# Optimization experiments

Hardware: AMD Instinct MI355X
Metric: run time of the kernel (lower is better)

Reference implementation:

```python
import jax, jax.numpy as jnp
import numpy as np

N, E, F_IN = 50000, 800000, 128
H1, C1 = 4, 32          # layer 1: heads, channels (concat -> 128)
H2, C2 = 1, 40          # layer 2: out heads, num_class (mean over heads)
NEG_SLOPE = 0.2


def setup_inputs() -> dict:
    key = jax.random.key(0)
    ks = jax.random.split(key, 10)
    x = jax.random.normal(ks[0], (N, F_IN), dtype=jnp.float32)
    edge_index = jax.random.randint(ks[1], (2, E), 0, N, dtype=jnp.int32)
    s1 = 1.0 / np.sqrt(F_IN)
    s2 = 1.0 / np.sqrt(H1 * C1)
    W1 = jax.random.normal(ks[2], (F_IN, H1 * C1), dtype=jnp.float32) * s1
    att_src1 = jax.random.normal(ks[3], (H1, C1), dtype=jnp.float32) * s1
    att_dst1 = jax.random.normal(ks[4], (H1, C1), dtype=jnp.float32) * s1
    b1 = jnp.zeros((H1 * C1,), dtype=jnp.float32)
    W2 = jax.random.normal(ks[5], (H1 * C1, H2 * C2), dtype=jnp.float32) * s2
    att_src2 = jax.random.normal(ks[6], (H2, C2), dtype=jnp.float32) * s2
    att_dst2 = jax.random.normal(ks[7], (H2, C2), dtype=jnp.float32) * s2
    b2 = jnp.zeros((C2,), dtype=jnp.float32)
    return {"x": x, "edge_index": edge_index, "W1": W1, "att_src1": att_src1,
            "att_dst1": att_dst1, "b1": b1, "W2": W2, "att_src2": att_src2,
            "att_dst2": att_dst2, "b2": b2}


def _gat_layer(x, src, dst, W, a_src, a_dst, b, concat):
    # PyG GATConv (eval): linear -> per-head attention logits on edges ->
    # segment-softmax over each destination's in-edges -> scatter-aggregate.
    n = x.shape[0]
    Hh, C = a_src.shape
    h = (x @ W).reshape(n, Hh, C)                       # [N,H,C]
    al_s = jnp.sum(h * a_src, axis=-1)                  # [N,H]
    al_d = jnp.sum(h * a_dst, axis=-1)                  # [N,H]
    alpha = jax.nn.leaky_relu(al_s[src] + al_d[dst], NEG_SLOPE)  # [E,H]
    m = jax.lax.stop_gradient(jax.ops.segment_max(alpha, dst, num_segments=n))
    e = jnp.exp(alpha - m[dst])
    denom = jax.ops.segment_sum(e, dst, num_segments=n)
    a = e / (denom[dst] + 1e-16)                        # [E,H]
    out = jax.ops.segment_sum(h[src] * a[..., None], dst, num_segments=n)
    out = out.reshape(n, Hh * C) if concat else out.mean(axis=1)
    return out + b


def reference(x, edge_index, W1, att_src1, att_dst1, b1, W2, att_src2, att_dst2, b2):
    n = x.shape[0]
    loop = jnp.arange(n, dtype=edge_index.dtype)        # GATConv add_self_loops=True
    src = jnp.concatenate([edge_index[0], loop])
    dst = jnp.concatenate([edge_index[1], loop])
    h = _gat_layer(x, src, dst, W1, att_src1, att_dst1, b1, concat=True)
    h = jax.nn.elu(h)
    out = _gat_layer(h, src, dst, W2, att_src2, att_dst2, b2, concat=False)
    return out
```

## Files before the change

kernel.cpp:

```cpp
#include <hip/hip_runtime.h>
#include <hip/hip_bf16.h>
#include <hip/hip_fp16.h>
#include <math.h>

constexpr int N_NODES = 50000;
constexpr int E_EDGES = 800000;
constexpr float NEG_SLOPE = 0.2f;
constexpr int CAP = 64;
constexpr int G1_BLOCKS   = (N_NODES + 63) / 64;
constexpr int LINK_CHUNKS = (E_EDGES + 2047) / 2048;
constexpr int LINK_BLOCKS = LINK_CHUNKS * 8;
constexpr int RANGE_SZ    = N_NODES / 8;

typedef _Float16 half8 __attribute__((ext_vector_type(8)));
typedef _Float16 half2v __attribute__((ext_vector_type(2)));
typedef float    floatx4 __attribute__((ext_vector_type(4)));

static inline int cdiv(long long a, int b) { return (int)((a + b - 1) / b); }

__device__ inline float leaky(float a) { return a > 0.f ? a : NEG_SLOPE * a; }
__device__ inline unsigned pack2h(float a, float b) {
    union { _Float16 h[2]; unsigned u; } p;
    p.h[0] = (_Float16)a; p.h[1] = (_Float16)b; return p.u;
}
__device__ inline float2 unp2h(unsigned u) {
    __half2 hh = *reinterpret_cast<__half2*>(&u);
    return __half22float2(hh);
}
__device__ inline float sel4(const float4& v, int h) {
    float a = (h & 2) ? v.z : v.x;
    float b = (h & 2) ? v.w : v.y;
    return (h & 1) ? b : a;
}

__global__ __launch_bounds__(256) void prep_kernel(const float* __restrict__ W1,
                                                   const float* __restrict__ W2,
                                                   int* __restrict__ deg,
                                                   _Float16* __restrict__ w1t,
                                                   _Float16* __restrict__ w2t) {
    int b = blockIdx.x, t = threadIdx.x;
    if (b < 196) {
        int i = b * 256 + t;
        if (i < N_NODES) deg[i] = 0;
        return;
    }
    if (b < 196 + 64) {
        int idx = (b - 196) * 256 + t;
        int k = idx >> 7, c = idx & 127;
        w1t[c * 128 + k] = (_Float16)W1[k * 128 + c];
        return;
    }
    {
        int idx = (b - 260) * 256 + t;
        int k = idx / 40, c = idx - k * 40;
        w2t[c * 128 + k] = (_Float16)W2[k * 40 + c];
    }
}

__global__ __launch_bounds__(256, 8) void gemm1_link_kernel(const float* __restrict__ x,
                                                            const _Float16* __restrict__ w1t,
                                                            const float* __restrict__ as1,
                                                            const float* __restrict__ ad1,
                                                            unsigned short* __restrict__ h1h,
                                                            float* __restrict__ als,
                                                            float* __restrict__ ald,
                                                            const int* __restrict__ ei,
                                                            int* __restrict__ deg,
                                                            unsigned short* __restrict__ csr16) {
    __shared__ _Float16 xS[64 * 136];
    __shared__ float asld[128], adld[128];
    int t = threadIdx.x;

    if (blockIdx.x >= G1_BLOCKS) {
        int lb    = blockIdx.x - G1_BLOCKS;
        int range = lb & 7;
        int chunk = lb >> 3;
        int e0    = chunk * 2048 + t * 8;
        if (e0 < E_EDGES) {
            int4 sa = *(const int4*)&ei[e0];
            int4 sb = *(const int4*)&ei[e0 + 4];
            int4 da = *(const int4*)&ei[E_EDGES + e0];
            int4 db = *(const int4*)&ei[E_EDGES + e0 + 4];
            int ss[8] = { sa.x, sa.y, sa.z, sa.w, sb.x, sb.y, sb.z, sb.w };
            int dd[8] = { da.x, da.y, da.z, da.w, db.x, db.y, db.z, db.w };
            int dlo = range * RANGE_SZ, dhi = dlo + RANGE_SZ;
            #pragma unroll
            for (int j = 0; j < 8; ++j) {
                if (dd[j] >= dlo && dd[j] < dhi) {
                    int slot = atomicAdd(&deg[dd[j]], 1) + 1;
                    if (slot < CAP) csr16[dd[j] * CAP + slot] = (unsigned short)ss[j];
                }
            }
        }
        return;
    }

    int row0 = blockIdx.x * 64;
    if (t < 128) { asld[t] = as1[t]; adld[t] = ad1[t]; }
    #pragma unroll
    for (int i = 0; i < 8; ++i) {
        int fi = i * 256 + t;
        int r = fi >> 5, c4 = (fi & 31) * 4;
        int gr = row0 + r;
        float4 v = make_float4(0.f, 0.f, 0.f, 0.f);
        if (gr < N_NODES) v = *(const float4*)&x[(size_t)gr * 128 + c4];
        union { _Float16 h[4]; uint2 u; } pk;
        pk.h[0] = (_Float16)v.x; pk.h[1] = (_Float16)v.y;
        pk.h[2] = (_Float16)v.z; pk.h[3] = (_Float16)v.w;
        *(uint2*)&xS[r * 136 + c4] = pk.u;
    }
    __syncthreads();

    int w = t >> 6, lane = t & 63, quad = lane >> 4, l16 = lane & 15;
    floatx4 z = {0.f, 0.f, 0.f, 0.f};
    floatx4 c[4][2];
    #pragma unroll
    for (int rt = 0; rt < 4; ++rt) { c[rt][0] = z; c[rt][1] = z; }

    const _Float16* wt0 = w1t + (size_t)(w * 32 + l16) * 128;
    const _Float16* wt1 = wt0 + 16 * 128;
    #pragma unroll
    for (int ks = 0; ks < 4; ++ks) {
        int kg = ks * 32 + quad * 8;
        half8 b0 = *(const half8*)&wt0[kg];
        half8 b1 = *(const half8*)&wt1[kg];
        #pragma unroll
        for (int rt = 0; rt < 4; ++rt) {
            half8 a = *(const half8*)&xS[(rt * 16 + l16) * 136 + kg];
            c[rt][0] = __builtin_amdgcn_mfma_f32_16x16x32_f16(a, b0, c[rt][0], 0, 0, 0);
            c[rt][1] = __builtin_amdgcn_mfma_f32_16x16x32_f16(a, b1, c[rt][1], 0, 0, 0);
        }
    }
    __syncthreads();
    _Float16* cbuf = xS;
    #pragma unroll
    for (int rt = 0; rt < 4; ++rt)
        #pragma unroll
        for (int ctl = 0; ctl < 2; ++ctl)
            #pragma unroll
            for (int reg = 0; reg < 4; ++reg)
                cbuf[(rt * 16 + quad * 4 + reg) * 136 + (w * 32 + ctl * 16 + l16)]
                    = (_Float16)c[rt][ctl][reg];
    __syncthreads();
    int r = t >> 2, hq = t & 3;
    int n = row0 + r;
    if (n < N_NODES) {
        if (hq == 0) csr16[n * CAP] = (unsigned short)n;
        float ps = 0.f, pd = 0.f;
        #pragma unroll
        for (int i = 0; i < 4; ++i) {
            uint4 uv = *(uint4*)&cbuf[r * 136 + hq * 32 + i * 8];
            *(uint4*)&h1h[(size_t)n * 128 + hq * 32 + i * 8] = uv;
            union { uint4 u; _Float16 h[8]; } cv; cv.u = uv;
            #pragma unroll
            for (int k = 0; k < 8; ++k) {
                float v = (float)cv.h[k];
                ps += v * asld[hq * 32 + i * 8 + k];
                pd += v * adld[hq * 32 + i * 8 + k];
            }
        }
        als[n * 4 + hq] = ps;
        ald[n * 4 + hq] = pd;
    }
}

__global__ __launch_bounds__(256) void agg1_kernel(const int* __restrict__ deg_,
                                                   const unsigned short* __restrict__ csr16,
                                                   const float* __restrict__ als,
                                                   const float4* __restrict__ ald4,
                                                   const unsigned short* __restrict__ h1h,
                                                   const float* __restrict__ b1,
                                                   unsigned short* __restrict__ out1h) {
    int wv   = threadIdx.x >> 6;
    int lane = threadIdx.x & 63;
    int half = lane >> 5;
    int l    = lane & 31;
    int myhead = l >> 3;
    int we   = lane & 15;
    int wh   = lane >> 4;
    int d    = blockIdx.x * 4 + wv;
    int dg   = min(deg_[d] + 1, CAP);
    int base = d * CAP;
    float4 aldd = ald4[d];
    float d_hw = sel4(aldd, wh);

    float sm = 0.f;
    float acc[4] = {0.f, 0.f, 0.f, 0.f};
    int sfirst = (int)csr16[base];
    #pragma unroll 2
    for (int j = 0; j < dg; j += 16) {
        int s_w = (int)csr16[base + j + we];
        float av = als[s_w * 4 + wh];
        float wgt = (j + we < dg) ? __expf(leaky(av + d_hw)) : 0.f;
        uint4 blkA = *(const uint4*)&csr16[base + j];
        uint4 blkB = *(const uint4*)&csr16[base + j + 8];
        unsigned bw[8] = { blkA.x, blkA.y, blkA.z, blkA.w,
                           blkB.x, blkB.y, blkB.z, blkB.w };
        int ss[8];
        #pragma unroll
        for (int p = 0; p < 8; ++p) {
            unsigned b = __builtin_amdgcn_readfirstlane(bw[p]);
            int e0 = (int)(b & 0xffff), e1 = (int)(b >> 16);
            int mys = half ? e1 : e0;
            if (j + 2 * p + half >= dg) mys = sfirst;
            ss[p] = mys;
        }
        uint2 hv[8];
        #pragma unroll
        for (int p = 0; p < 8; ++p)
            hv[p] = *(const uint2*)(h1h + ((size_t)ss[p] << 7) + 4 * l);
        float ww[8];
        #pragma unroll
        for (int p = 0; p < 8; ++p) {
            ww[p] = __shfl(wgt, 16 * myhead + 2 * p + half);
            sm += ww[p];
        }
        half2v hacc0 = { (_Float16)0.f, (_Float16)0.f };
        half2v hacc1 = { (_Float16)0.f, (_Float16)0.f };
        #pragma unroll
        for (int p = 0; p < 8; ++p) {
            half2v v0 = *reinterpret_cast<half2v*>(&hv[p].x);
            half2v v1 = *reinterpret_cast<half2v*>(&hv[p].y);
            _Float16 hw = (_Float16)ww[p];
            half2v hwv = { hw, hw };
            hacc0 += v0 * hwv;
            hacc1 += v1 * hwv;
        }
        acc[0] += (float)hacc0[0]; acc[1] += (float)hacc0[1];
        acc[2] += (float)hacc1[0]; acc[3] += (float)hacc1[1];
    }
    sm += __shfl_xor(sm, 32);
    #pragma unroll
    for (int k = 0; k < 4; ++k) acc[k] += __shfl_xor(acc[k], 32);
    if (half == 0) {
        float inv = 1.f / (sm + 1e-16f);
        float v[4];
        #pragma unroll
        for (int k = 0; k < 4; ++k) {
            v[k] = acc[k] * inv + b1[4 * l + k];
            v[k] = v[k] > 0.f ? v[k] : __expf(v[k]) - 1.f;
        }
        uint2 o;
        o.x = pack2h(v[0], v[1]);
        o.y = pack2h(v[2], v[3]);
        *(uint2*)&out1h[(size_t)d * 128 + 4 * l] = o;
    }
}

__global__ __launch_bounds__(256, 8) void gemm2_kernel(const unsigned short* __restrict__ out1h,
                                                       const _Float16* __restrict__ w2t,
                                                       const float* __restrict__ as2,
                                                       const float* __restrict__ ad2,
                                                       unsigned short* __restrict__ h2h,
                                                       float* __restrict__ als,
                                                       float* __restrict__ ald) {
    __shared__ _Float16 aS[64 * 136];
    __shared__ float asld[40], adld[40];
    int t = threadIdx.x;
    int row0 = blockIdx.x * 64;
    if (t < 40) { asld[t] = as2[t]; adld[t] = ad2[t]; }
    #pragma unroll
    for (int i = 0; i < 4; ++i) {
        int fi = i * 256 + t;
        int r = fi >> 4, s8 = (fi & 15) * 8;
        int gr = row0 + r;
        uint4 v = make_uint4(0u, 0u, 0u, 0u);
        if (gr < N_NODES) v = *(const uint4*)&out1h[(size_t)gr * 128 + s8];
        *(uint4*)&aS[r * 136 + s8] = v;
    }
    __syncthreads();

    int w = t >> 6, lane = t & 63, quad = lane >> 4, l16 = lane & 15;
    floatx4 z = {0.f, 0.f, 0.f, 0.f};
    floatx4 c0 = z, c1 = z, c2 = z;
    int n2 = (l16 < 8) ? 32 + l16 : 39;
    const _Float16* wb0 = w2t + (size_t)l16 * 128;
    const _Float16* wb1 = w2t + (size_t)(16 + l16) * 128;
    const _Float16* wb2 = w2t + (size_t)n2 * 128;
    #pragma unroll
    for (int ks = 0; ks < 4; ++ks) {
        int kg = ks * 32 + quad * 8;
        half8 b0 = *(const half8*)&wb0[kg];
        half8 b1 = *(const half8*)&wb1[kg];
        half8 b2 = *(const half8*)&wb2[kg];
        half8 a  = *(const half8*)&aS[(w * 16 + l16) * 136 + kg];
        c0 = __builtin_amdgcn_mfma_f32_16x16x32_f16(a, b0, c0, 0, 0, 0);
        c1 = __builtin_amdgcn_mfma_f32_16x16x32_f16(a, b1, c1, 0, 0, 0);
        c2 = __builtin_amdgcn_mfma_f32_16x16x32_f16(a, b2, c2, 0, 0, 0);
    }
    __syncthreads();
    #pragma unroll
    for (int reg = 0; reg < 4; ++reg) {
        int rr = (w * 16 + quad * 4 + reg) * 136;
        aS[rr + l16]      = (_Float16)c0[reg];
        aS[rr + 16 + l16] = (_Float16)c1[reg];
        aS[rr + 32 + l16] = (_Float16)c2[reg];
    }
    __syncthreads();
    for (int fi = t; fi < 320; fi += 256) {
        int r = fi / 5, s = fi - r * 5;
        int n = row0 + r;
        if (n < N_NODES) {
            uint4 v = *(uint4*)&aS[r * 136 + s * 8];
            *(uint4*)&h2h[(size_t)n * 40 + s * 8] = v;
        }
    }
    int r = t >> 2, q = t & 3;
    int n = row0 + r;
    float ps = 0.f, pd = 0.f;
    #pragma unroll
    for (int i = 0; i < 10; ++i) {
        int cc = q * 10 + i;
        float v = (float)aS[r * 136 + cc];
        ps += v * asld[cc]; pd += v * adld[cc];
    }
    ps += __shfl_xor(ps, 1); ps += __shfl_xor(ps, 2);
    pd += __shfl_xor(pd, 1); pd += __shfl_xor(pd, 2);
    if (q == 0 && n < N_NODES) { als[n] = ps; ald[n] = pd; }
}

__global__ __launch_bounds__(256) void agg2_kernel(const int* __restrict__ deg_,
                                                   const unsigned short* __restrict__ csr16,
                                                   const float* __restrict__ als,
                                                   const float* __restrict__ ald,
                                                   const unsigned short* __restrict__ h2h,
                                                   const float* __restrict__ b2,
                                                   float* __restrict__ out) {
    int wv   = threadIdx.x >> 6;
    int lane = threadIdx.x & 63;
    int d    = blockIdx.x * 4 + wv;
    int dg   = min(deg_[d] + 1, CAP);
    int base = d * CAP;
    float aldd = ald[d];

    int slot = lane / 20;
    int idx  = lane - slot * 20;
    int sfirst = (int)csr16[base];
    float sm = 0.f, acc0 = 0.f, acc1 = 0.f;
    if (lane < 60) {
        #pragma unroll 2
        for (int jb = 0; jb < dg; jb += 12) {
            int ss[4]; unsigned hv[4]; float ww[4];
            #pragma unroll
            for (int i = 0; i < 4; ++i) {
                int jj = jb + slot + 3 * i;
                ss[i] = (jj < dg) ? (int)csr16[base + jj] : sfirst;
            }
            #pragma unroll
            for (int i = 0; i < 4; ++i)
                hv[i] = *(const unsigned*)(h2h + (size_t)ss[i] * 40 + 2 * idx);
            #pragma unroll
            for (int i = 0; i < 4; ++i) {
                int jj = jb + slot + 3 * i;
                float w = __expf(leaky(als[ss[i]] + aldd));
                ww[i] = (jj < dg) ? w : 0.f;
            }
            #pragma unroll
            for (int i = 0; i < 4; ++i) {
                float2 f = unp2h(hv[i]);
                acc0 += f.x * ww[i]; acc1 += f.y * ww[i]; sm += ww[i];
            }
        }
    }
    float s1 = __shfl(sm,   idx + 20), s2 = __shfl(sm,   idx + 40);
    float t0 = __shfl(acc0, idx + 20), t1 = __shfl(acc0, idx + 40);
    float u0 = __shfl(acc1, idx + 20), u1 = __shfl(acc1, idx + 40);
    sm += s1 + s2; acc0 += t0 + t1; acc1 += u0 + u1;
    if (lane < 20) {
        float inv = 1.f / (sm + 1e-16f);
        float2 o = make_float2(acc0 * inv + b2[2 * lane], acc1 * inv + b2[2 * lane + 1]);
        *(float2*)&out[(size_t)d * 40 + 2 * lane] = o;
    }
}

constexpr size_t OFF_H1H    = 0;
constexpr size_t OFF_OUT1   = 3200000;
constexpr size_t OFF_ALS1   = 6400000;
constexpr size_t OFF_ALD1   = 6600000;
constexpr size_t OFF_W1T    = 6800000;
constexpr size_t OFF_W2T    = 6808192;
constexpr size_t OFF_DEG    = 6860000;
constexpr size_t OFF_CSRF   = 6920000;
constexpr size_t WS_FLOATS  = 10120000;

extern "C" void kernel_launch(void* const* d_in, const int* in_sizes, int n_in,
                              void* d_out, int out_size, void* d_ws, size_t ws_size,
                              hipStream_t stream) {
    const float* x   = (const float*)d_in[0];
    const int*   ei  = (const int*)  d_in[1];
    const float* W1  = (const float*)d_in[2];
    const float* as1 = (const float*)d_in[3];
    const float* ad1 = (const float*)d_in[4];
    const float* b1  = (const float*)d_in[5];
    const float* W2  = (const float*)d_in[6];
    const float* as2 = (const float*)d_in[7];
    const float* ad2 = (const float*)d_in[8];
    const float* b2  = (const float*)d_in[9];
    float* out = (float*)d_out;

    if (ws_size < WS_FLOATS * sizeof(float)) return;

    float* ws = (float*)d_ws;
    unsigned short* h1h   = (unsigned short*)(ws + OFF_H1H);
    unsigned short* h2h   = (unsigned short*)(ws + OFF_H1H);
    unsigned short* out1h = (unsigned short*)(ws + OFF_OUT1);
    float* als1    = ws + OFF_ALS1;
    float* ald1    = ws + OFF_ALD1;
    float* als2    = ws + OFF_ALS1;
    float* ald2    = ws + OFF_ALD1;
    _Float16* w1t  = (_Float16*)(ws + OFF_W1T);
    _Float16* w2t  = (_Float16*)(ws + OFF_W2T);
    int*   deg     = (int*)(ws + OFF_DEG);
    unsigned short* csr16 = (unsigned short*)(ws + OFF_CSRF);

    prep_kernel<<<280, 256, 0, stream>>>(W1, W2, deg, w1t, w2t);
    gemm1_link_kernel<<<G1_BLOCKS + LINK_BLOCKS, 256, 0, stream>>>(
        x, w1t, as1, ad1, h1h, als1, ald1, ei, deg, csr16);

    agg1_kernel<<<N_NODES / 4, 256, 0, stream>>>(deg, csr16, als1,
                                                 (const float4*)ald1,
                                                 h1h, b1, out1h);

    gemm2_kernel<<<cdiv(N_NODES, 64), 256, 0, stream>>>(out1h, w2t, as2, ad2, h2h, als2, ald2);
    agg2_kernel<<<N_NODES / 4, 256, 0, stream>>>(deg, csr16, als2, ald2, h2h, b2, out);
}
```

Before: 203.7 us.

## Fuse layer-1 aggregation with layer-2 GEMM through shared memory

Merges agg1 and gemm2 into one kernel with 1024-thread blocks. Sixteen waves each aggregate four destination rows into a shared-memory tile, then four waves run the MFMA GEMM on that tile and write h2 plus the attention logits. This drops the out1 round-trip through global memory and one kernel launch. In exchange, workspace buffers are re-laid out so h2/als2/ald2 no longer alias layer-1 data, 12 of 16 waves sit idle during the GEMM, and the large blocks may lower occupancy and balance for the gather phase.

```diff
diff --git a/kernel.cpp b/kernel.cpp
--- a/kernel.cpp
+++ b/kernel.cpp
@@ -164,159 +164,157 @@
     }
 }
 
-__global__ __launch_bounds__(256) void agg1_kernel(const int* __restrict__ deg_,
-                                                   const unsigned short* __restrict__ csr16,
-                                                   const float* __restrict__ als,
-                                                   const float4* __restrict__ ald4,
-                                                   const unsigned short* __restrict__ h1h,
-                                                   const float* __restrict__ b1,
-                                                   unsigned short* __restrict__ out1h) {
-    int wv   = threadIdx.x >> 6;
-    int lane = threadIdx.x & 63;
+__global__ __launch_bounds__(1024, 8) void agg1_gemm2_kernel(const int* __restrict__ deg_,
+                                                             const unsigned short* __restrict__ csr16,
+                                                             const float* __restrict__ als,
+                                                             const float4* __restrict__ ald4,
+                                                             const unsigned short* __restrict__ h1h,
+                                                             const float* __restrict__ b1,
+                                                             const _Float16* __restrict__ w2t,
+                                                             const float* __restrict__ as2,
+                                                             const float* __restrict__ ad2,
+                                                             unsigned short* __restrict__ h2h,
+                                                             float* __restrict__ als2,
+                                                             float* __restrict__ ald2) {
+    __shared__ _Float16 aS[64 * 136];
+    __shared__ float asld[40], adld[40];
+    int t = threadIdx.x;
+    int wv   = t >> 6;
+    int lane = t & 63;
+    if (t < 40) { asld[t] = as2[t]; adld[t] = ad2[t]; }
+    int row0 = blockIdx.x * 64;
     int half = lane >> 5;
     int l    = lane & 31;
     int myhead = l >> 3;
     int we   = lane & 15;
     int wh   = lane >> 4;
-    int d    = blockIdx.x * 4 + wv;
-    int dg   = min(deg_[d] + 1, CAP);
-    int base = d * CAP;
-    float4 aldd = ald4[d];
-    float d_hw = sel4(aldd, wh);
-
-    float sm = 0.f;
-    float acc[4] = {0.f, 0.f, 0.f, 0.f};
-    int sfirst = (int)csr16[base];
-    #pragma unroll 2
-    for (int j = 0; j < dg; j += 16) {
-        int s_w = (int)csr16[base + j + we];
-        float av = als[s_w * 4 + wh];
-        float wgt = (j + we < dg) ? __expf(leaky(av + d_hw)) : 0.f;
-        uint4 blkA = *(const uint4*)&csr16[base + j];
-        uint4 blkB = *(const uint4*)&csr16[base + j + 8];
-        unsigned bw[8] = { blkA.x, blkA.y, blkA.z, blkA.w,
-                           blkB.x, blkB.y, blkB.z, blkB.w };
-        int ss[8];
-        #pragma unroll
-        for (int p = 0; p < 8; ++p) {
-            unsigned b = __builtin_amdgcn_readfirstlane(bw[p]);
-            int e0 = (int)(b & 0xffff), e1 = (int)(b >> 16);
-            int mys = half ? e1 : e0;
-            if (j + 2 * p + half >= dg) mys = sfirst;
-            ss[p] = mys;
-        }
-        uint2 hv[8];
-        #pragma unroll
-        for (int p = 0; p < 8; ++p)
-            hv[p] = *(const uint2*)(h1h + ((size_t)ss[p] << 7) + 4 * l);
-        float ww[8];
-        #pragma unroll
-        for (int p = 0; p < 8; ++p) {
-            ww[p] = __shfl(wgt, 16 * myhead + 2 * p + half);
-            sm += ww[p];
-        }
-        half2v hacc0 = { (_Float16)0.f, (_Float16)0.f };
-        half2v hacc1 = { (_Float16)0.f, (_Float16)0.f };
-        #pragma unroll
-        for (int p = 0; p < 8; ++p) {
-            half2v v0 = *reinterpret_cast<half2v*>(&hv[p].x);
-            half2v v1 = *reinterpret_cast<half2v*>(&hv[p].y);
-            _Float16 hw = (_Float16)ww[p];
-            half2v hwv = { hw, hw };
-            hacc0 += v0 * hwv;
-            hacc1 += v1 * hwv;
-        }
-        acc[0] += (float)hacc0[0]; acc[1] += (float)hacc0[1];
-        acc[2] += (float)hacc1[0]; acc[3] += (float)hacc1[1];
-    }
-    sm += __shfl_xor(sm, 32);
-    #pragma unroll
-    for (int k = 0; k < 4; ++k) acc[k] += __shfl_xor(acc[k], 32);
-    if (half == 0) {
-        float inv = 1.f / (sm + 1e-16f);
-        float v[4];
-        #pragma unroll
-        for (int k = 0; k < 4; ++k) {
-            v[k] = acc[k] * inv + b1[4 * l + k];
-            v[k] = v[k] > 0.f ? v[k] : __expf(v[k]) - 1.f;
-        }
-        uint2 o;
-        o.x = pack2h(v[0], v[1]);
-        o.y = pack2h(v[2], v[3]);
-        *(uint2*)&out1h[(size_t)d * 128 + 4 * l] = o;
-    }
-}
-
-__global__ __launch_bounds__(256, 8) void gemm2_kernel(const unsigned short* __restrict__ out1h,
-                                                       const _Float16* __restrict__ w2t,
-                                                       const float* __restrict__ as2,
-                                                       const float* __restrict__ ad2,
-                                                       unsigned short* __restrict__ h2h,
-                                                       float* __restrict__ als,
-                                                       float* __restrict__ ald) {
-    __shared__ _Float16 aS[64 * 136];
-    __shared__ float asld[40], adld[40];
-    int t = threadIdx.x;
-    int row0 = blockIdx.x * 64;
-    if (t < 40) { asld[t] = as2[t]; adld[t] = ad2[t]; }
-    #pragma unroll
-    for (int i = 0; i < 4; ++i) {
-        int fi = i * 256 + t;
-        int r = fi >> 4, s8 = (fi & 15) * 8;
-        int gr = row0 + r;
-        uint4 v = make_uint4(0u, 0u, 0u, 0u);
-        if (gr < N_NODES) v = *(const uint4*)&out1h[(size_t)gr * 128 + s8];
-        *(uint4*)&aS[r * 136 + s8] = v;
+
+    for (int jd = 0; jd < 4; ++jd) {
+        int tr = wv * 4 + jd;
+        int d  = row0 + tr;
+        if (d < N_NODES) {
+            int dg   = min(deg_[d] + 1, CAP);
+            int base = d * CAP;
+            float4 aldd = ald4[d];
+            float d_hw = sel4(aldd, wh);
+            float sm = 0.f;
+            float acc[4] = {0.f, 0.f, 0.f, 0.f};
+            int sfirst = (int)csr16[base];
+            #pragma unroll 2
+            for (int j = 0; j < dg; j += 16) {
+                int s_w = (int)csr16[base + j + we];
+                float av = als[s_w * 4 + wh];
+                float wgt = (j + we < dg) ? __expf(leaky(av + d_hw)) : 0.f;
+                uint4 blkA = *(const uint4*)&csr16[base + j];
+                uint4 blkB = *(const uint4*)&csr16[base + j + 8];
+                unsigned bw[8] = { blkA.x, blkA.y, blkA.z, blkA.w,
+                                   blkB.x, blkB.y, blkB.z, blkB.w };
+                int ss[8];
+                #pragma unroll
+                for (int p = 0; p < 8; ++p) {
+                    unsigned b = __builtin_amdgcn_readfirstlane(bw[p]);
+                    int e0 = (int)(b & 0xffff), e1 = (int)(b >> 16);
+                    int mys = half ? e1 : e0;
+                    if (j + 2 * p + half >= dg) mys = sfirst;
+                    ss[p] = mys;
+                }
+                uint2 hv[8];
+                #pragma unroll
+                for (int p = 0; p < 8; ++p)
+                    hv[p] = *(const uint2*)(h1h + ((size_t)ss[p] << 7) + 4 * l);
+                float ww[8];
+                #pragma unroll
+                for (int p = 0; p < 8; ++p) {
+                    ww[p] = __shfl(wgt, 16 * myhead + 2 * p + half);
+                    sm += ww[p];
+                }
+                half2v hacc0 = { (_Float16)0.f, (_Float16)0.f };
+                half2v hacc1 = { (_Float16)0.f, (_Float16)0.f };
+                #pragma unroll
+                for (int p = 0; p < 8; ++p) {
+                    half2v v0 = *reinterpret_cast<half2v*>(&hv[p].x);
+                    half2v v1 = *reinterpret_cast<half2v*>(&hv[p].y);
+                    _Float16 hw = (_Float16)ww[p];
+                    half2v hwv = { hw, hw };
+                    hacc0 += v0 * hwv;
+                    hacc1 += v1 * hwv;
+                }
+                acc[0] += (float)hacc0[0]; acc[1] += (float)hacc0[1];
+                acc[2] += (float)hacc1[0]; acc[3] += (float)hacc1[1];
+            }
+            sm += __shfl_xor(sm, 32);
+            #pragma unroll
+            for (int k = 0; k < 4; ++k) acc[k] += __shfl_xor(acc[k], 32);
+            if (half == 0) {
+                float inv = 1.f / (sm + 1e-16f);
+                float v[4];
+                #pragma unroll
+                for (int k = 0; k < 4; ++k) {
+                    v[k] = acc[k] * inv + b1[4 * l + k];
+                    v[k] = v[k] > 0.f ? v[k] : __expf(v[k]) - 1.f;
+                }
+                uint2 o;
+                o.x = pack2h(v[0], v[1]);
+                o.y = pack2h(v[2], v[3]);
+                *(uint2*)&aS[tr * 136 + 4 * l] = o;
+            }
+        } else if (half == 0) {
+            *(uint2*)&aS[tr * 136 + 4 * l] = make_uint2(0u, 0u);
+        }
     }
     __syncthreads();
 
-    int w = t >> 6, lane = t & 63, quad = lane >> 4, l16 = lane & 15;
-    floatx4 z = {0.f, 0.f, 0.f, 0.f};
-    floatx4 c0 = z, c1 = z, c2 = z;
-    int n2 = (l16 < 8) ? 32 + l16 : 39;
-    const _Float16* wb0 = w2t + (size_t)l16 * 128;
-    const _Float16* wb1 = w2t + (size_t)(16 + l16) * 128;
-    const _Float16* wb2 = w2t + (size_t)n2 * 128;
-    #pragma unroll
-    for (int ks = 0; ks < 4; ++ks) {
-        int kg = ks * 32 + quad * 8;
-        half8 b0 = *(const half8*)&wb0[kg];
-        half8 b1 = *(const half8*)&wb1[kg];
-        half8 b2 = *(const half8*)&wb2[kg];
-        half8 a  = *(const half8*)&aS[(w * 16 + l16) * 136 + kg];
-        c0 = __builtin_amdgcn_mfma_f32_16x16x32_f16(a, b0, c0, 0, 0, 0);
-        c1 = __builtin_amdgcn_mfma_f32_16x16x32_f16(a, b1, c1, 0, 0, 0);
-        c2 = __builtin_amdgcn_mfma_f32_16x16x32_f16(a, b2, c2, 0, 0, 0);
+    if (wv < 4) {
+        int w = wv, quad = lane >> 4, l16 = lane & 15;
+        floatx4 z = {0.f, 0.f, 0.f, 0.f};
+        floatx4 c0 = z, c1 = z, c2 = z;
+        int n2 = (l16 < 8) ? 32 + l16 : 39;
+        const _Float16* wb0 = w2t + (size_t)l16 * 128;
+        const _Float16* wb1 = w2t + (size_t)(16 + l16) * 128;
+        const _Float16* wb2 = w2t + (size_t)n2 * 128;
+        #pragma unroll
+        for (int ks = 0; ks < 4; ++ks) {
+            int kg = ks * 32 + quad * 8;
+            half8 b0 = *(const half8*)&wb0[kg];
+            half8 b1 = *(const half8*)&wb1[kg];
+            half8 b2 = *(const half8*)&wb2[kg];
+            half8 a  = *(const half8*)&aS[(w * 16 + l16) * 136 + kg];
+            c0 = __builtin_amdgcn_mfma_f32_16x16x32_f16(a, b0, c0, 0, 0, 0);
+            c1 = __builtin_amdgcn_mfma_f32_16x16x32_f16(a, b1, c1, 0, 0, 0);
+            c2 = __builtin_amdgcn_mfma_f32_16x16x32_f16(a, b2, c2, 0, 0, 0);
+        }
+        #pragma unroll
+        for (int reg = 0; reg < 4; ++reg) {
+            int rr = (w * 16 + quad * 4 + reg) * 136;
+            aS[rr + l16]      = (_Float16)c0[reg];
+            aS[rr + 16 + l16] = (_Float16)c1[reg];
+            aS[rr + 32 + l16] = (_Float16)c2[reg];
+        }
     }
     __syncthreads();
-    #pragma unroll
-    for (int reg = 0; reg < 4; ++reg) {
-        int rr = (w * 16 + quad * 4 + reg) * 136;
-        aS[rr + l16]      = (_Float16)c0[reg];
-        aS[rr + 16 + l16] = (_Float16)c1[reg];
-        aS[rr + 32 + l16] = (_Float16)c2[reg];
-    }
-    __syncthreads();
-    for (int fi = t; fi < 320; fi += 256) {
-        int r = fi / 5, s = fi - r * 5;
+
+    if (t < 320) {
+        int r = t / 5, s = t - r * 5;
         int n = row0 + r;
         if (n < N_NODES) {
             uint4 v = *(uint4*)&aS[r * 136 + s * 8];
             *(uint4*)&h2h[(size_t)n * 40 + s * 8] = v;
         }
     }
-    int r = t >> 2, q = t & 3;
-    int n = row0 + r;
-    float ps = 0.f, pd = 0.f;
-    #pragma unroll
-    for (int i = 0; i < 10; ++i) {
-        int cc = q * 10 + i;
-        float v = (float)aS[r * 136 + cc];
-        ps += v * asld[cc]; pd += v * adld[cc];
-    }
-    ps += __shfl_xor(ps, 1); ps += __shfl_xor(ps, 2);
-    pd += __shfl_xor(pd, 1); pd += __shfl_xor(pd, 2);
-    if (q == 0 && n < N_NODES) { als[n] = ps; ald[n] = pd; }
+    if (t < 256) {
+        int r = t >> 2, q = t & 3;
+        int n = row0 + r;
+        float ps = 0.f, pd = 0.f;
+        #pragma unroll
+        for (int i = 0; i < 10; ++i) {
+            int cc = q * 10 + i;
+            float v = (float)aS[r * 136 + cc];
+            ps += v * asld[cc]; pd += v * adld[cc];
+        }
+        ps += __shfl_xor(ps, 1); ps += __shfl_xor(ps, 2);
+        pd += __shfl_xor(pd, 1); pd += __shfl_xor(pd, 2);
+        if (q == 0 && n < N_NODES) { als2[n] = ps; ald2[n] = pd; }
+    }
 }
 
 __global__ __launch_bounds__(256) void agg2_kernel(const int* __restrict__ deg_,
@@ -374,13 +372,15 @@
 }
 
 constexpr size_t OFF_H1H    = 0;
-constexpr size_t OFF_OUT1   = 3200000;
+constexpr size_t OFF_H2H    = 3200000;
 constexpr size_t OFF_ALS1   = 6400000;
 constexpr size_t OFF_ALD1   = 6600000;
 constexpr size_t OFF_W1T    = 6800000;
 constexpr size_t OFF_W2T    = 6808192;
 constexpr size_t OFF_DEG    = 6860000;
 constexpr size_t OFF_CSRF   = 6920000;
+constexpr size_t OFF_ALS2   = 8520000;
+constexpr size_t OFF_ALD2   = 8570000;
 constexpr size_t WS_FLOATS  = 10120000;
 
 extern "C" void kernel_launch(void* const* d_in, const int* in_sizes, int n_in,
@@ -402,12 +402,11 @@
 
     float* ws = (float*)d_ws;
     unsigned short* h1h   = (unsigned short*)(ws + OFF_H1H);
-    unsigned short* h2h   = (unsigned short*)(ws + OFF_H1H);
-    unsigned short* out1h = (unsigned short*)(ws + OFF_OUT1);
+    unsigned short* h2h   = (unsigned short*)(ws + OFF_H2H);
     float* als1    = ws + OFF_ALS1;
     float* ald1    = ws + OFF_ALD1;
-    float* als2    = ws + OFF_ALS1;
-    float* ald2    = ws + OFF_ALD1;
+    float* als2    = ws + OFF_ALS2;
+    float* ald2    = ws + OFF_ALD2;
     _Float16* w1t  = (_Float16*)(ws + OFF_W1T);
     _Float16* w2t  = (_Float16*)(ws + OFF_W2T);
     int*   deg     = (int*)(ws + OFF_DEG);
@@ -417,10 +416,9 @@
     gemm1_link_kernel<<<G1_BLOCKS + LINK_BLOCKS, 256, 0, stream>>>(
         x, w1t, as1, ad1, h1h, als1, ald1, ei, deg, csr16);
 
-    agg1_kernel<<<N_NODES / 4, 256, 0, stream>>>(deg, csr16, als1,
-                                                 (const float4*)ald1,
-                                                 h1h, b1, out1h);
-
-    gemm2_kernel<<<cdiv(N_NODES, 64), 256, 0, stream>>>(out1h, w2t, as2, ad2, h2h, als2, ald2);
+    agg1_gemm2_kernel<<<cdiv(N_NODES, 64), 1024, 0, stream>>>(
+        deg, csr16, als1, (const float4*)ald1, h1h, b1,
+        w2t, as2, ad2, h2h, als2, ald2);
+
     agg2_kernel<<<N_NODES / 4, 256, 0, stream>>>(deg, csr16, als2, ald2, h2h, b2, out);
 }
```

After: 210.5 us. +3.3%, slower.
